# Kernel tuning notes

Measured on AMD Instinct MI355X. Metric: run time of the kernel, lower is better.

Reference implementation:

```python
import jax, jax.numpy as jnp
import numpy as np

N_WIRES = 4
N_LAYERS = 3
EPS = 1e-5


def _rx(t):
    c = jnp.cos(t / 2).astype(jnp.complex64)
    s = jnp.sin(t / 2).astype(jnp.complex64)
    return jnp.stack([jnp.stack([c, -1j * s], -1), jnp.stack([-1j * s, c], -1)], -2)


def _ry(t):
    c = jnp.cos(t / 2).astype(jnp.complex64)
    s = jnp.sin(t / 2).astype(jnp.complex64)
    return jnp.stack([jnp.stack([c, -s], -1), jnp.stack([s, c], -1)], -2)


def _rz(t):
    e0 = jnp.exp(-1j * t.astype(jnp.complex64) / 2)
    e1 = jnp.exp(1j * t.astype(jnp.complex64) / 2)
    z = jnp.zeros_like(e0)
    return jnp.stack([jnp.stack([e0, z], -1), jnp.stack([z, e1], -1)], -2)


def _apply_1q(st, U, w, n=N_WIRES):
    # st: [B, 2^n]; U: [2,2] (shared) or [B,2,2] (per-sample)
    B = st.shape[0]
    a, c = 2 ** w, 2 ** (n - w - 1)
    st = st.reshape(B, a, 2, c)
    if U.ndim == 2:
        st = jnp.einsum('ij,bajc->baic', U, st)
    else:
        st = jnp.einsum('bij,bajc->baic', U, st)
    return st.reshape(B, -1)


def _apply_cnot(st, w, n=N_WIRES):
    # CNOT with control w, target w+1
    B = st.shape[0]
    a, c = 2 ** w, 2 ** (n - w - 2)
    st = st.reshape(B, a, 2, 2, c)
    st = jnp.stack([st[:, :, 0], jnp.flip(st[:, :, 1], axis=2)], axis=2)
    return st.reshape(B, -1)


def _expz(st, w, n=N_WIRES):
    B = st.shape[0]
    a, c = 2 ** w, 2 ** (n - w - 1)
    p = (st.real ** 2 + st.imag ** 2).reshape(B, a, 2, c)
    return (p[:, :, 0] - p[:, :, 1]).sum(axis=(1, 2))


def _circuit(vparams, feats):
    # feats: [B, n_wires] encoding angles; vparams: [L, n_wires, 3]
    B = feats.shape[0]
    st = jnp.zeros((B, 2 ** N_WIRES), jnp.complex64).at[:, 0].set(1.0)
    for w in range(N_WIRES):
        st = _apply_1q(st, _rx(feats[:, w]), w)
    for l in range(N_LAYERS):
        for w in range(N_WIRES):
            st = _apply_1q(st, _rx(vparams[l, w, 0]), w)
            st = _apply_1q(st, _ry(vparams[l, w, 1]), w)
            st = _apply_1q(st, _rz(vparams[l, w, 2]), w)
        for w in range(N_WIRES - 1):
            st = _apply_cnot(st, w)
    return jnp.stack([_expz(st, w) for w in range(N_WIRES)], axis=1)  # [B, n_wires]


def setup_inputs() -> dict:
    key = jax.random.key(0)
    ks = jax.random.split(key, 4)
    B = 65536
    x = jax.random.normal(ks[0], (B, 1, 28, 28), jnp.float32)
    W = jax.random.normal(ks[1], (16, N_WIRES), jnp.float32) * 0.25
    b = jax.random.normal(ks[2], (N_WIRES,), jnp.float32) * 0.1
    vparams = jax.random.normal(ks[3], (N_LAYERS, N_WIRES, 3), jnp.float32)
    gamma = jnp.ones((N_WIRES,), jnp.float32)
    beta = jnp.zeros((N_WIRES,), jnp.float32)
    return {"x": x, "W": W, "b": b, "vparams": vparams, "gamma": gamma, "beta": beta}


def reference(x, W, b, vparams, gamma, beta):
    B = x.shape[0]
    # avg_pool2d kernel=6 stride=6 on 28x28 -> 4x4 (floor mode drops last 4 rows/cols)
    pooled = x[:, :, :24, :24].reshape(B, 1, 4, 6, 4, 6).mean(axis=(3, 5))
    feats = pooled.reshape(B, 16) @ W + b  # [B, n_wires]
    out = _circuit(vparams, feats)  # [B, n_wires]
    # BatchNorm1d (training mode: biased batch stats)
    mu = out.mean(axis=0)
    var = out.var(axis=0)
    return (out - mu) / jnp.sqrt(var + EPS) * gamma + beta
```

## Files before the change

kernel.cpp:

```cpp
#include <hip/hip_runtime.h>
#include <math.h>


#define IMG_PER_BLOCK 16
#define IMG_F 784
#define IMG_F4_USED 168
#define USED_F 672
#define TOT4 (IMG_PER_BLOCK * IMG_F4_USED)
#define ACC_SETS 64

__global__ __launch_bounds__(256) void qfc_prep(
    const float* __restrict__ vparams,
    float2* __restrict__ Ucg)
{
    const int t = threadIdx.x;
    const int j = t >> 4, i = t & 15;
    float ux = (i == j) ? 1.f : 0.f, uy = 0.f;
    for (int l = 0; l < 3; ++l) {
        for (int w = 0; w < 4; ++w) {
            const float* vp = vparams + (l * 4 + w) * 3;
            const int m = 8 >> w;
            float s, c;
            __sincosf(0.5f * vp[0], &s, &c);
            {
                float ox = __shfl_xor(ux, m);
                float oy = __shfl_xor(uy, m);
                float nx = c * ux + s * oy;
                float ny = c * uy - s * ox;
                ux = nx; uy = ny;
            }
            __sincosf(0.5f * vp[1], &s, &c);
            {
                float ox = __shfl_xor(ux, m);
                float oy = __shfl_xor(uy, m);
                float sg = (i & m) ? s : -s;
                ux = c * ux + sg * ox;
                uy = c * uy + sg * oy;
            }
            __sincosf(0.5f * vp[2], &s, &c);
            {
                float sg = (i & m) ? s : -s;
                float nx = ux * c - sg * uy;
                float ny = uy * c + sg * ux;
                ux = nx; uy = ny;
            }
        }
        for (int w = 0; w < 3; ++w) {
            int mc = 8 >> w, mt = 4 >> w;
            float ox = __shfl_xor(ux, mt);
            float oy = __shfl_xor(uy, mt);
            if (i & mc) { ux = ox; uy = oy; }
        }
    }
    int pc = __popc(j) & 3;
    float px, py;
    if (pc == 0)      { px =  ux; py =  uy; }
    else if (pc == 1) { px =  uy; py = -ux; }
    else if (pc == 2) { px = -ux; py = -uy; }
    else              { px = -uy; py =  ux; }
    Ucg[t] = make_float2(px, py);
}

__global__ __launch_bounds__(256) void qfc_main(
    const float* __restrict__ x,
    const float* __restrict__ W,
    const float* __restrict__ bias,
    const float2* __restrict__ Ucg,
    float* __restrict__ out,
    double* __restrict__ acc,
    int B)
{
    __shared__ float  lds_img[IMG_PER_BLOCK * USED_F];
    __shared__ float2 Uc[256];
    __shared__ float  pooled_s[256];
    __shared__ float  bsum[4], bsq[4];

    const int t   = threadIdx.x;
    const int blk = blockIdx.x;

    if (t < 4) { bsum[t] = 0.f; bsq[t] = 0.f; }
    Uc[t] = Ucg[t];

    {
        const float4* x4   = (const float4*)x;
        float4*       lds4 = (float4*)lds_img;
        #pragma unroll
        for (int k = 0; k < 11; ++k) {
            int q = t + k * 256;
            if (q < TOT4) {
                int g   = q / IMG_F4_USED;
                int r4  = q - g * IMG_F4_USED;
                int img = blk * IMG_PER_BLOCK + g;
                if (img < B) lds4[q] = x4[img * (IMG_F / 4) + r4];
            }
        }
    }
    __syncthreads();

    {
        const int g = t >> 4, cell = t & 15;
        const int ci = cell >> 2, cj = cell & 3;
        const float* base = lds_img + g * USED_F + ci * 6 * 28 + cj * 6;
        float sum = 0.f;
        #pragma unroll
        for (int r = 0; r < 6; ++r) {
            const float2* p2 = (const float2*)(base + r * 28);
            float2 a = p2[0], b2 = p2[1], c2 = p2[2];
            sum += a.x + a.y + b2.x + b2.y + c2.x + c2.y;
        }
        pooled_s[t] = sum * (1.0f / 36.0f);
    }
    __syncthreads();

    {
        const int g = t >> 4, i = t & 15;
        const float* pl = pooled_s + g * 16;
        float f0 = bias[0], f1 = bias[1], f2 = bias[2], f3 = bias[3];
        #pragma unroll
        for (int k = 0; k < 16; ++k) {
            float p = pl[k];
            f0 += p * W[k * 4 + 0];
            f1 += p * W[k * 4 + 1];
            f2 += p * W[k * 4 + 2];
            f3 += p * W[k * 4 + 3];
        }
        float c0, s0, c1, s1, c2, s2, c3, s3;
        __sincosf(0.5f * f0, &s0, &c0);
        __sincosf(0.5f * f1, &s1, &c1);
        __sincosf(0.5f * f2, &s2, &c2);
        __sincosf(0.5f * f3, &s3, &c3);
        float AB[4] = { c0 * c1, c0 * s1, s0 * c1, s0 * s1 };
        float CD[4] = { c2 * c3, c2 * s3, s2 * c3, s2 * s3 };
        float yx = 0.f, yy = 0.f;
        #pragma unroll
        for (int j = 0; j < 16; ++j) {
            float r = AB[j >> 2] * CD[j & 3];
            float2 u = Uc[j * 16 + i];
            yx += u.x * r;
            yy += u.y * r;
        }
        float q = yx * yx + yy * yy;
        #pragma unroll
        for (int d = 1; d <= 8; d <<= 1) {
            float o = __shfl_xor(q, d);
            q = (i & d) ? (o - q) : (o + q);
        }
        int img = blk * IMG_PER_BLOCK + g;
        if ((i == 1 || i == 2 || i == 4 || i == 8) && img < B) {
            int w = (i == 8) ? 0 : (i == 4) ? 1 : (i == 2) ? 2 : 3;
            out[img * 4 + w] = q;
            atomicAdd(&bsum[w], q);
            atomicAdd(&bsq[w],  q * q);
        }
    }
    __syncthreads();

    if (t < 4) {
        int s = blk & (ACC_SETS - 1);
        atomicAdd(&acc[s * 8 + t],     (double)bsum[t]);
        atomicAdd(&acc[s * 8 + 4 + t], (double)bsq[t]);
    }
}

__global__ __launch_bounds__(256) void qfc_bn(
    float* __restrict__ out,
    const double* __restrict__ acc,
    const float* __restrict__ gamma,
    const float* __restrict__ beta,
    int B)
{
    __shared__ double tot_s[8];
    __shared__ float  mu_s[4], sc_s[4], bt_s[4];
    const int t = threadIdx.x;
    if (t < 8) {
        double tot = 0.0;
        for (int s = 0; s < ACC_SETS; ++s) tot += acc[s * 8 + t];
        tot_s[t] = tot;
    }
    __syncthreads();
    if (t < 4) {
        double invB = 1.0 / (double)B;
        double mu   = tot_s[t] * invB;
        double var  = tot_s[4 + t] * invB - mu * mu;
        mu_s[t] = (float)mu;
        sc_s[t] = (float)(1.0 / sqrt(var + 1e-5)) * gamma[t];
        bt_s[t] = beta[t];
    }
    __syncthreads();
    int idx = blockIdx.x * blockDim.x + t;
    if (idx < B) {
        float4* o4 = (float4*)out;
        float4 v = o4[idx];
        v.x = (v.x - mu_s[0]) * sc_s[0] + bt_s[0];
        v.y = (v.y - mu_s[1]) * sc_s[1] + bt_s[1];
        v.z = (v.z - mu_s[2]) * sc_s[2] + bt_s[2];
        v.w = (v.w - mu_s[3]) * sc_s[3] + bt_s[3];
        o4[idx] = v;
    }
}

extern "C" void kernel_launch(void* const* d_in, const int* in_sizes, int n_in,
                              void* d_out, int out_size, void* d_ws, size_t ws_size,
                              hipStream_t stream) {
    const float* x       = (const float*)d_in[0];
    const float* W       = (const float*)d_in[1];
    const float* b       = (const float*)d_in[2];
    const float* vparams = (const float*)d_in[3];
    const float* gamma   = (const float*)d_in[4];
    const float* beta    = (const float*)d_in[5];
    float* out = (float*)d_out;
    const int B = in_sizes[0] / IMG_F;

    double* acc = (double*)d_ws;
    float2* Ucg = (float2*)((char*)d_ws + ACC_SETS * 8 * sizeof(double));

    hipMemsetAsync(acc, 0, ACC_SETS * 8 * sizeof(double), stream);
    qfc_prep<<<1, 256, 0, stream>>>(vparams, Ucg);

    int nblk1 = (B + IMG_PER_BLOCK - 1) / IMG_PER_BLOCK;
    qfc_main<<<nblk1, 256, 0, stream>>>(x, W, b, Ucg, out, acc, B);

    int nblk2 = (B + 255) / 256;
    qfc_bn<<<nblk2, 256, 0, stream>>>(out, acc, gamma, beta, B);
}
```

Baseline: 300.5 us.

## Load only the used 24 columns per row, pool via shuffles, fold memset into prep

The image staging now fetches only the 6 float4s per row that the pooling uses (24 of 28 columns) instead of the 24 full rows. This cuts global reads and LDS footprint per block. The pooled values are passed between lanes with warp shuffles rather than a shared array plus a barrier. The accumulator zeroing moves from a separate memset into the prep kernel, removing one stream operation. The strided row loads are less contiguous than the previous streaming copy, which could hurt coalescing somewhat.

```diff
diff --git a/kernel.cpp b/kernel.cpp
--- a/kernel.cpp
+++ b/kernel.cpp
@@ -4,16 +4,21 @@
 
 #define IMG_PER_BLOCK 16
 #define IMG_F 784
-#define IMG_F4_USED 168
-#define USED_F 672
-#define TOT4 (IMG_PER_BLOCK * IMG_F4_USED)
+#define IMG_F4 196
+#define ROW_F4 6
+#define STG_F4 144
+#define STG_F 576
+#define TOT4 (IMG_PER_BLOCK * STG_F4)
 #define ACC_SETS 64
 
 __global__ __launch_bounds__(256) void qfc_prep(
     const float* __restrict__ vparams,
-    float2* __restrict__ Ucg)
+    float2* __restrict__ Ucg,
+    double* __restrict__ acc)
 {
     const int t = threadIdx.x;
+    acc[t] = 0.0;
+    acc[t + 256] = 0.0;
     const int j = t >> 4, i = t & 15;
     float ux = (i == j) ? 1.f : 0.f, uy = 0.f;
     for (int l = 0; l < 3; ++l) {
@@ -70,9 +75,8 @@
     double* __restrict__ acc,
     int B)
 {
-    __shared__ float  lds_img[IMG_PER_BLOCK * USED_F];
+    __shared__ float  lds_img[IMG_PER_BLOCK * STG_F];
     __shared__ float2 Uc[256];
-    __shared__ float  pooled_s[256];
     __shared__ float  bsum[4], bsq[4];
 
     const int t   = threadIdx.x;
@@ -85,40 +89,40 @@
         const float4* x4   = (const float4*)x;
         float4*       lds4 = (float4*)lds_img;
         #pragma unroll
-        for (int k = 0; k < 11; ++k) {
-            int q = t + k * 256;
-            if (q < TOT4) {
-                int g   = q / IMG_F4_USED;
-                int r4  = q - g * IMG_F4_USED;
-                int img = blk * IMG_PER_BLOCK + g;
-                if (img < B) lds4[q] = x4[img * (IMG_F / 4) + r4];
-            }
-        }
-    }
-    __syncthreads();
-
+        for (int k = 0; k < 9; ++k) {
+            int q    = t + k * 256;
+            int g    = q / STG_F4;
+            int r4   = q - g * STG_F4;
+            int row  = r4 / ROW_F4;
+            int col4 = r4 - row * ROW_F4;
+            int img  = blk * IMG_PER_BLOCK + g;
+            if (img < B)
+                lds4[q] = x4[img * IMG_F4 + row * 7 + col4];
+        }
+    }
+    __syncthreads();
+
+    float pv;
     {
         const int g = t >> 4, cell = t & 15;
         const int ci = cell >> 2, cj = cell & 3;
-        const float* base = lds_img + g * USED_F + ci * 6 * 28 + cj * 6;
+        const float* base = lds_img + g * STG_F + ci * 6 * 24 + cj * 6;
         float sum = 0.f;
         #pragma unroll
         for (int r = 0; r < 6; ++r) {
-            const float2* p2 = (const float2*)(base + r * 28);
+            const float2* p2 = (const float2*)(base + r * 24);
             float2 a = p2[0], b2 = p2[1], c2 = p2[2];
             sum += a.x + a.y + b2.x + b2.y + c2.x + c2.y;
         }
-        pooled_s[t] = sum * (1.0f / 36.0f);
-    }
-    __syncthreads();
+        pv = sum * (1.0f / 36.0f);
+    }
 
     {
         const int g = t >> 4, i = t & 15;
-        const float* pl = pooled_s + g * 16;
         float f0 = bias[0], f1 = bias[1], f2 = bias[2], f3 = bias[3];
         #pragma unroll
         for (int k = 0; k < 16; ++k) {
-            float p = pl[k];
+            float p = __shfl(pv, (t & 48) | k, 64);
             f0 += p * W[k * 4 + 0];
             f1 += p * W[k * 4 + 1];
             f2 += p * W[k * 4 + 2];
@@ -214,8 +218,7 @@
     double* acc = (double*)d_ws;
     float2* Ucg = (float2*)((char*)d_ws + ACC_SETS * 8 * sizeof(double));
 
-    hipMemsetAsync(acc, 0, ACC_SETS * 8 * sizeof(double), stream);
-    qfc_prep<<<1, 256, 0, stream>>>(vparams, Ucg);
+    qfc_prep<<<1, 256, 0, stream>>>(vparams, Ucg, acc);
 
     int nblk1 = (B + IMG_PER_BLOCK - 1) / IMG_PER_BLOCK;
     qfc_main<<<nblk1, 256, 0, stream>>>(x, W, b, Ucg, out, acc, B);
```

After: 293.0 us. -2.5%, faster.
